# Kernel optimization log

Hardware: AMD Instinct MI355X
Metric: run time of the kernel (lower is better)

## Reference

```python
import jax, jax.numpy as jnp
import numpy as np

B, S, HID, NH, HD = 2, 2048, 1024, 16, 64  # batch, seq, hidden, heads, head_dim (1024//NH)
ROPE_THETA = 10000.0
EPS = 1e-5


def _ternary_quantize(w):
    # BitNet b1.58 absmean weight quantization: ternary values + scalar scale.
    s = jnp.mean(jnp.abs(w)) + EPS
    q = jnp.clip(jnp.round(w / s), -1.0, 1.0)
    return q, s


def _rotate_half(x):
    x1, x2 = jnp.split(x, 2, axis=-1)
    return jnp.concatenate((-x2, x1), axis=-1)


def _rope_cos_sin(position_ids, head_dim, dtype):
    inv_freq = 1.0 / (ROPE_THETA ** (jnp.arange(0, head_dim, 2, dtype=jnp.float32) / head_dim))
    freqs = position_ids.astype(jnp.float32)[..., None] * inv_freq  # [b, s, hd/2]
    emb = jnp.concatenate((freqs, freqs), axis=-1)  # [b, s, hd]
    # add head axis -> [b, 1, s, hd]
    return jnp.cos(emb)[:, None].astype(dtype), jnp.sin(emb)[:, None].astype(dtype)


def setup_inputs() -> dict:
    key = jax.random.key(0)
    ks = jax.random.split(key, 5)
    hidden_states = jax.random.normal(ks[0], (B, S, HID), jnp.float32)
    hidden_states_scale = jnp.ones((1,), jnp.float32)
    position_ids = jnp.broadcast_to(jnp.arange(S, dtype=jnp.int32), (B, S))
    wq = jax.random.normal(ks[1], (HID, HID), jnp.float32) * 0.02
    wk = jax.random.normal(ks[2], (HID, HID), jnp.float32) * 0.02
    wv = jax.random.normal(ks[3], (HID, HID), jnp.float32) * 0.02
    wo = jax.random.normal(ks[4], (HID, HID), jnp.float32) * 0.02
    return {"hidden_states": hidden_states, "hidden_states_scale": hidden_states_scale,
            "position_ids": position_ids, "wq": wq, "wk": wk, "wv": wv, "wo": wo}


def reference(hidden_states, hidden_states_scale, position_ids, wq, wk, wv, wo):
    b, s, _ = hidden_states.shape
    hs_scale = hidden_states_scale.reshape(())

    # QuantizedLinear: ternary weight values, scale carried separately.
    wq_q, sq = _ternary_quantize(wq)
    wk_q, sk = _ternary_quantize(wk)
    wv_q, sv = _ternary_quantize(wv)
    wo_q, so = _ternary_quantize(wo)

    # Projections in the quantized-value domain: out = x @ Wq^T, out_scale = x_scale * w_scale
    q = jnp.einsum('bsh,oh->bso', hidden_states, wq_q)
    k = jnp.einsum('bsh,oh->bso', hidden_states, wk_q)
    v = jnp.einsum('bsh,oh->bso', hidden_states, wv_q)
    q_scale = hs_scale * sq
    k_scale = hs_scale * sk
    v_scale = hs_scale * sv

    # [b, nh, s, hd]
    q = q.reshape(b, s, NH, HD).transpose(0, 2, 1, 3)
    k = k.reshape(b, s, NH, HD).transpose(0, 2, 1, 3)
    v = v.reshape(b, s, NH, HD).transpose(0, 2, 1, 3)

    cos, sin = _rope_cos_sin(position_ids, HD, q.dtype)
    q = q * cos + _rotate_half(q) * sin
    k = k * cos + _rotate_half(k) * sin

    # quantized_matmul(Q, qs, K, ks): values multiply, scales multiply (scale unused by softmax,
    # matching the original which softmaxes the quantized-domain scores).
    attn = jnp.einsum('bhqd,bhkd->bhqk', q, k).astype(jnp.float32) * (1.0 / np.sqrt(HD))
    attn = jax.nn.softmax(attn, axis=-1)

    # quantized_matmul(attn, 1.0, V, vs)
    out = jnp.einsum('bhqk,bhkd->bhqd', attn, v.astype(jnp.float32))
    out_scale = 1.0 * v_scale

    out = out.transpose(0, 2, 1, 3).reshape(b, s, HID)
    out = jnp.einsum('bsh,oh->bso', out, wo_q)
    out_scale = out_scale * so
    return out, out_scale
```

## Files before the change

### kernel.cpp

```cpp
#include <hip/hip_runtime.h>
#include <hip/hip_bf16.h>

#define NB 2
#define NS 2048
#define NHID 1024
#define NHEAD 16
#define NHD 64
#define NTOK (NB*NS)
#define WELEM (NHID*NHID)

typedef unsigned short u16;
typedef __attribute__((ext_vector_type(4))) float floatx4;
typedef __attribute__((ext_vector_type(16))) float floatx16;
typedef __attribute__((ext_vector_type(8))) __bf16 bf16x8;
typedef __attribute__((ext_vector_type(8))) unsigned short ushort8;
typedef __attribute__((ext_vector_type(4))) unsigned short ushort4v;
typedef __attribute__((ext_vector_type(2))) unsigned uint2v;

__device__ __forceinline__ u16 f2bf(float f) {
  union { float f; unsigned u; } a; a.f = f;
  unsigned u = a.u;
  unsigned r = (u + 0x7fffu + ((u >> 16) & 1u)) >> 16;
  return (u16)r;
}
__device__ __forceinline__ float bf2f(u16 s) {
  union { unsigned u; float f; } a; a.u = ((unsigned)s) << 16;
  return a.f;
}
__device__ __forceinline__ void gload16(const void* g, void* lds) {
  __builtin_amdgcn_global_load_lds(
      (const __attribute__((address_space(1))) unsigned int*)g,
      (__attribute__((address_space(3))) unsigned int*)lds, 16, 0, 0);
}
__device__ __forceinline__ uint2v pl32(unsigned a, unsigned b) {
  return __builtin_amdgcn_permlane32_swap(a, b, false, false);
}
__device__ __forceinline__ float mergemax(float x) {
  uint2v r = pl32(__float_as_uint(x), __float_as_uint(x));
  return fmaxf(__uint_as_float(r[0]), __uint_as_float(r[1]));
}
__device__ __forceinline__ float mergesum(float x) {
  uint2v r = pl32(__float_as_uint(x), __float_as_uint(x));
  return __uint_as_float(r[0]) + __uint_as_float(r[1]);
}
__device__ __forceinline__ float tmax16(const floatx16& v) {
  float a = fmaxf(fmaxf(fmaxf(v[0], v[1]), fmaxf(v[2], v[3])),
                  fmaxf(fmaxf(v[4], v[5]), fmaxf(v[6], v[7])));
  float b = fmaxf(fmaxf(fmaxf(v[8], v[9]), fmaxf(v[10], v[11])),
                  fmaxf(fmaxf(v[12], v[13]), fmaxf(v[14], v[15])));
  return fmaxf(a, b);
}

__global__ void k_init(double* sums) { if (threadIdx.x < 4) sums[threadIdx.x] = 0.0; }

__global__ void k_abssum(const float* __restrict__ wq, const float* __restrict__ wk,
                         const float* __restrict__ wv, const float* __restrict__ wo,
                         double* __restrict__ sums) {
  const float* srcs[4] = {wq, wk, wv, wo};
  const float* w = srcs[blockIdx.y];
  int idx = (blockIdx.x * 256 + threadIdx.x) * 16;
  float s = 0.f;
#pragma unroll
  for (int j = 0; j < 4; j++) {
    float4 v = *(const float4*)(w + idx + j * 4);
    s += fabsf(v.x) + fabsf(v.y) + fabsf(v.z) + fabsf(v.w);
  }
#pragma unroll
  for (int off = 32; off; off >>= 1) s += __shfl_down(s, off);
  __shared__ float ps[4];
  if ((threadIdx.x & 63) == 0) ps[threadIdx.x >> 6] = s;
  __syncthreads();
  if (threadIdx.x == 0) atomicAdd(&sums[blockIdx.y], (double)(ps[0] + ps[1] + ps[2] + ps[3]));
}

__global__ void k_quantsplit(const float* __restrict__ wq, const float* __restrict__ wk,
                             const float* __restrict__ wv, const float* __restrict__ wo,
                             const double* __restrict__ sums, u16* __restrict__ wt,
                             const float* __restrict__ x,
                             u16* __restrict__ xh, u16* __restrict__ xl) {
  int bid = blockIdx.x;
  if (bid < 4096) {
    const float* srcs[4] = {wq, wk, wv, wo};
    int y = bid >> 10, xb = bid & 1023;
    const float* w = srcs[y];
    u16* dst = wt + y * WELEM;
    float s = (float)(sums[y] / (double)WELEM) + 1e-5f;
    int idx = (xb * 256 + threadIdx.x) * 4;
    float4 v = *(const float4*)(w + idx);
    float f[4] = {v.x, v.y, v.z, v.w};
    union { u16 ss[4]; uint2 u; } O;
#pragma unroll
    for (int j = 0; j < 4; j++) {
      float q = rintf(f[j] / s);
      q = fminf(1.f, fmaxf(-1.f, q));
      O.ss[j] = f2bf(q);
    }
    *(uint2*)(dst + idx) = O.u;
  } else {
    int idx = ((bid - 4096) * 256 + threadIdx.x) * 4;
    float4 v = *(const float4*)(x + idx);
    float f[4] = {v.x, v.y, v.z, v.w};
    union { u16 s[4]; uint2 u; } H, L;
#pragma unroll
    for (int j = 0; j < 4; j++) {
      u16 hb = f2bf(f[j]);
      H.s[j] = hb;
      L.s[j] = f2bf(f[j] - bf2f(hb));
    }
    *(uint2*)(xh + idx) = H.u;
    *(uint2*)(xl + idx) = L.u;
  }
}

template <int MODE>
__global__ __launch_bounds__(256) void k_gemm(
    const u16* __restrict__ Ahi, const u16* __restrict__ Alo,
    const u16* __restrict__ Wt, float* __restrict__ outf,
    u16* __restrict__ qh, u16* __restrict__ ql,
    u16* __restrict__ kh, u16* __restrict__ kl,
    u16* __restrict__ vt) {
  constexpr int BUF = (MODE == 0) ? 24576 : 16384;
  __shared__ __attribute__((aligned(16))) char GSM[2 * BUF];
  const int tid = threadIdx.x;
  const int wave = tid >> 6, lane = tid & 63;
  const int lr = lane & 15, lh = lane >> 4;
  const int bm = blockIdx.x, bn = blockIdx.y, z = blockIdx.z;
  const u16* W = Wt + (MODE == 0 ? z : 3) * WELEM;
  const int wr = wave >> 1, wc = wave & 1;

  floatx4 acc[4][4];
#pragma unroll
  for (int i = 0; i < 4; i++)
#pragma unroll
    for (int j = 0; j < 4; j++) acc[i][j] = (floatx4){0.f, 0.f, 0.f, 0.f};

  const int e0 = tid * 8;
  const int row0 = e0 >> 5, col0 = e0 & 31;

  auto stage = [&](int k0, int nb) {
#pragma unroll
    for (int it = 0; it < 2; ++it) {
      int row = row0 + it * 64;
      gload16(Ahi + (bm * 128 + row) * 1024 + k0 + col0, GSM + nb + it * 4096 + wave * 1024);
      if (MODE == 0)
        gload16(Alo + (bm * 128 + row) * 1024 + k0 + col0, GSM + nb + 8192 + it * 4096 + wave * 1024);
      gload16(W + (bn * 128 + row) * 1024 + k0 + col0,
              GSM + nb + (MODE == 0 ? 16384 : 8192) + it * 4096 + wave * 1024);
    }
  };

  stage(0, 0);

  for (int kt = 0; kt < 32; ++kt) {
    __syncthreads();
    const int cb = (kt & 1) * BUF;
    if (kt < 31) stage((kt + 1) * 32, ((kt + 1) & 1) * BUF);

    const u16* Ahp = (const u16*)(GSM + cb);
    const u16* Bp  = (const u16*)(GSM + cb + (MODE == 0 ? 16384 : 8192));
    bf16x8 ah[4], bfr[4];
#pragma unroll
    for (int mi = 0; mi < 4; mi++)
      ah[mi] = *(const bf16x8*)(Ahp + (wr * 64 + mi * 16 + lr) * 32 + lh * 8);
#pragma unroll
    for (int ni = 0; ni < 4; ni++)
      bfr[ni] = *(const bf16x8*)(Bp + (wc * 64 + ni * 16 + lr) * 32 + lh * 8);
#pragma unroll
    for (int mi = 0; mi < 4; mi++)
#pragma unroll
      for (int ni = 0; ni < 4; ni++)
        acc[mi][ni] = __builtin_amdgcn_mfma_f32_16x16x32_bf16(ah[mi], bfr[ni], acc[mi][ni], 0, 0, 0);
    if (MODE == 0) {
      const u16* Alp = (const u16*)(GSM + cb + 8192);
      bf16x8 al8[4];
#pragma unroll
      for (int mi = 0; mi < 4; mi++)
        al8[mi] = *(const bf16x8*)(Alp + (wr * 64 + mi * 16 + lr) * 32 + lh * 8);
#pragma unroll
      for (int mi = 0; mi < 4; mi++)
#pragma unroll
        for (int ni = 0; ni < 4; ni++)
          acc[mi][ni] = __builtin_amdgcn_mfma_f32_16x16x32_bf16(al8[mi], bfr[ni], acc[mi][ni], 0, 0, 0);
    }
  }

  if (MODE == 1) {
#pragma unroll
    for (int mi = 0; mi < 4; mi++)
#pragma unroll
      for (int ni = 0; ni < 4; ni++)
#pragma unroll
        for (int i = 0; i < 4; i++) {
          int row = bm * 128 + wr * 64 + mi * 16 + lh * 4 + i;
          int col = bn * 128 + wc * 64 + ni * 16 + lr;
          outf[row * 1024 + col] = acc[mi][ni][i];
        }
    return;
  }

  const int hh = bn * 2 + wc;
  if (z == 2) {
#pragma unroll
    for (int mi = 0; mi < 4; mi++) {
      int row0v = bm * 128 + wr * 64 + mi * 16 + lh * 4;
      int bb = row0v >> 11, s_ = row0v & 2047;
      size_t vbase = ((size_t)(bb * NHEAD + hh)) * (NHD * NS) + s_;
#pragma unroll
      for (int ni = 0; ni < 4; ni++) {
        int hd = ni * 16 + lr;
        union { u16 s4[4]; ushort4v v; } V4;
#pragma unroll
        for (int i = 0; i < 4; i++) V4.s4[i] = f2bf(acc[mi][ni][i]);
        *(ushort4v*)(vt + vbase + (size_t)hd * NS) = V4.v;
      }
    }
    return;
  }

  u16* dh = z ? kh : qh;
  u16* dl = z ? kl : ql;
#pragma unroll
  for (int mi = 0; mi < 4; mi++)
#pragma unroll
    for (int ni = 0; ni < 4; ni++)
#pragma unroll
      for (int i = 0; i < 4; i++) {
        int row = bm * 128 + wr * 64 + mi * 16 + lh * 4 + i;
        int hd = ni * 16 + lr;
        int bb = row >> 11, s_ = row & 2047;
        size_t dst = ((size_t)(bb * NHEAD + hh) * NS + s_) * NHD + hd;
        float v = acc[mi][ni][i];
        u16 hb = f2bf(v);
        dh[dst] = hb;
        dl[dst] = f2bf(v - bf2f(hb));
      }
}

__global__ void k_rope(const int* __restrict__ pos_ids,
                       u16* __restrict__ qh, u16* __restrict__ ql,
                       u16* __restrict__ kh, u16* __restrict__ kl) {
  int gid = blockIdx.x * 256 + threadIdx.x;
  int row = gid >> 5, d = gid & 31;
  int bh = row >> 11, s = row & 2047, b = bh >> 4;
  int pos = pos_ids[b * NS + s];
  float inv = exp2f((float)d * -0.4152410118609203f);
  float fr = (float)pos * inv;
  float c = cosf(fr), sn = sinf(fr);
  int off = row * 64 + d;
  {
    float x1 = bf2f(qh[off]) + bf2f(ql[off]);
    float x2 = bf2f(qh[off + 32]) + bf2f(ql[off + 32]);
    float n1 = x1 * c - x2 * sn;
    float n2 = x2 * c + x1 * sn;
    u16 h1 = f2bf(n1); qh[off] = h1;       ql[off] = f2bf(n1 - bf2f(h1));
    u16 h2 = f2bf(n2); qh[off + 32] = h2;  ql[off + 32] = f2bf(n2 - bf2f(h2));
  }
  {
    float x1 = bf2f(kh[off]) + bf2f(kl[off]);
    float x2 = bf2f(kh[off + 32]) + bf2f(kl[off + 32]);
    float n1 = x1 * c - x2 * sn;
    float n2 = x2 * c + x1 * sn;
    u16 h1 = f2bf(n1); kh[off] = h1;       kl[off] = f2bf(n1 - bf2f(h1));
    u16 h2 = f2bf(n2); kh[off + 32] = h2;  kl[off + 32] = f2bf(n2 - bf2f(h2));
  }
}

__global__ __launch_bounds__(512) void k_attn(
    const u16* __restrict__ qh, const u16* __restrict__ ql,
    const u16* __restrict__ kh, const u16* __restrict__ kl,
    const u16* __restrict__ vt, u16* __restrict__ aoh) {
  __shared__ __attribute__((aligned(16))) char SM[49152];
  const int tid = threadIdx.x, wave = tid >> 6, lane = tid & 63;
  const int l5 = lane & 31, hi = lane >> 5;
  const int bid = blockIdx.x;
  const int swzb = ((bid & 7) << 5) | (bid >> 3);
  const int qt = swzb & 7, bh = swzb >> 3;
  const int b = bh >> 4, hco = (bh & 15) * NHD;
  const int base = bh * (NS * NHD);
  const int qrow = qt * 256 + wave * 32 + l5;
  const float SC = 0.125f * 1.4426950408889634f;

  bf16x8 qfh[4], qfl[4];
#pragma unroll
  for (int s = 0; s < 4; s++) {
    int off = base + qrow * NHD + s * 16 + hi * 8;
    ushort8 hu = *(const ushort8*)(qh + off);
    ushort8 lu = *(const ushort8*)(ql + off);
    union { ushort8 u; bf16x8 v; } H, L;
#pragma unroll
    for (int j = 0; j < 8; j++) {
      float f = (bf2f(hu[j]) + bf2f(lu[j])) * SC;
      u16 hb = f2bf(f);
      H.u[j] = hb; L.u[j] = f2bf(f - bf2f(hb));
    }
    qfh[s] = H.v; qfl[s] = L.v;
  }

  const floatx16 Z16 = {};
  floatx16 acco[2];
  acco[0] = Z16; acco[1] = Z16;
  float m_r = -1e30f, l_r = 0.f;

  const char* khg0 = (const char*)(kh + base);
  const char* klg0 = (const char*)(kl + base);
  const char* vtg0 = (const char*)(vt + base);

#define STAGE_KV(key0_, nb_)                                                     \
  {                                                                              \
    const char* khg = khg0 + (key0_) * 128;                                      \
    const char* klg = klg0 + (key0_) * 128;                                      \
    const char* vtg = vtg0 + (key0_) * 2;                                        \
    int L = tid * 16;                                                            \
    int r7 = (L >> 7) & 7;                                                       \
    int g = L ^ (r7 << 4);                                                       \
    gload16(khg + g, SM + (nb_) + wave * 1024);                                  \
    gload16(klg + g, SM + (nb_) + 8192 + wave * 1024);                           \
    int vcol = (L & 127) ^ (r7 << 4);                                            \
    gload16(vtg + (size_t)(L >> 7) * 4096 + vcol,                                \
            SM + (nb_) + 16384 + wave * 1024);                                   \
  }

  STAGE_KV(0, 0);

  for (int kt = 0; kt < 32; ++kt) {
    __syncthreads();
    const int cb = (kt & 1) * 24576;
    const int key0 = kt * 64;

    if (kt < 31) STAGE_KV(key0 + 64, ((kt + 1) & 1) * 24576);

    floatx16 sacc[2];
#pragma unroll
    for (int t = 0; t < 2; t++) {
      const int row = 32 * t + l5;
      const int swz = (row & 7) << 4;
      {
        int byt = cb + row * 128 + ((hi * 16) ^ swz);
        bf16x8 ah = *(const bf16x8*)(SM + byt);
        bf16x8 al8 = *(const bf16x8*)(SM + 8192 + byt);
        __builtin_amdgcn_s_setprio(1);
        sacc[t] = __builtin_amdgcn_mfma_f32_32x32x16_bf16(ah, qfh[0], Z16, 0, 0, 0);
        sacc[t] = __builtin_amdgcn_mfma_f32_32x32x16_bf16(ah, qfl[0], sacc[t], 0, 0, 0);
        sacc[t] = __builtin_amdgcn_mfma_f32_32x32x16_bf16(al8, qfh[0], sacc[t], 0, 0, 0);
        __builtin_amdgcn_s_setprio(0);
      }
#pragma unroll
      for (int s = 1; s < 4; s++) {
        int byt = cb + row * 128 + ((s * 32 + hi * 16) ^ swz);
        bf16x8 ah = *(const bf16x8*)(SM + byt);
        bf16x8 al8 = *(const bf16x8*)(SM + 8192 + byt);
        __builtin_amdgcn_s_setprio(1);
        sacc[t] = __builtin_amdgcn_mfma_f32_32x32x16_bf16(ah, qfh[s], sacc[t], 0, 0, 0);
        sacc[t] = __builtin_amdgcn_mfma_f32_32x32x16_bf16(ah, qfl[s], sacc[t], 0, 0, 0);
        sacc[t] = __builtin_amdgcn_mfma_f32_32x32x16_bf16(al8, qfh[s], sacc[t], 0, 0, 0);
        __builtin_amdgcn_s_setprio(0);
      }
    }

    float mt = fmaxf(tmax16(sacc[0]), tmax16(sacc[1]));
    mt = mergemax(mt);
    if (!__all(mt <= m_r + 8.0f)) {
      float mn = fmaxf(m_r, mt);
      float sc2 = exp2f(m_r - mn);
      l_r *= sc2;
#pragma unroll
      for (int dt = 0; dt < 2; dt++)
#pragma unroll
        for (int r = 0; r < 16; r++) acco[dt][r] *= sc2;
      m_r = mn;
    }
    float s0 = 0.f, s1 = 0.f, s2 = 0.f, s3 = 0.f;
#pragma unroll
    for (int t = 0; t < 2; t++)
#pragma unroll
      for (int r = 0; r < 16; r += 4) {
        float p0 = exp2f(sacc[t][r + 0] - m_r);
        float p1 = exp2f(sacc[t][r + 1] - m_r);
        float p2 = exp2f(sacc[t][r + 2] - m_r);
        float p3 = exp2f(sacc[t][r + 3] - m_r);
        sacc[t][r + 0] = p0; sacc[t][r + 1] = p1;
        sacc[t][r + 2] = p2; sacc[t][r + 3] = p3;
        s0 += p0; s1 += p1; s2 += p2; s3 += p3;
      }
    l_r += mergesum((s0 + s1) + (s2 + s3));

    bf16x8 vtf[2][4];
#pragma unroll
    for (int dt = 0; dt < 2; dt++) {
      const int vrow = l5 + 32 * dt;
      const int swzv = (vrow & 7) << 4;
#pragma unroll
      for (int s = 0; s < 4; s++)
        vtf[dt][s] = *(const bf16x8*)(SM + cb + 16384 + vrow * 128 + ((s * 32 + hi * 16) ^ swzv));
    }

#pragma unroll
    for (int s = 0; s < 4; s++) {
      int t = s >> 1, rb = (s & 1) * 8;
      union { __bf16 bb[8]; unsigned u[4]; } Wp;
#pragma unroll
      for (int j = 0; j < 8; j++) Wp.bb[j] = (__bf16)sacc[t][rb + j];
      uint2v r02 = pl32(Wp.u[0], Wp.u[2]);
      uint2v r13 = pl32(Wp.u[1], Wp.u[3]);
      union { unsigned u[4]; bf16x8 v; } P;
      P.u[0] = r02[0]; P.u[1] = r13[0]; P.u[2] = r02[1]; P.u[3] = r13[1];
      __builtin_amdgcn_s_setprio(1);
      acco[0] = __builtin_amdgcn_mfma_f32_32x32x16_bf16(vtf[0][s], P.v, acco[0], 0, 0, 0);
      acco[1] = __builtin_amdgcn_mfma_f32_32x32x16_bf16(vtf[1][s], P.v, acco[1], 0, 0, 0);
      __builtin_amdgcn_s_setprio(0);
    }
  }

  float inv = 1.0f / l_r;
  float* OT = (float*)SM;
#pragma unroll
  for (int rnd = 0; rnd < 2; rnd++) {
    __syncthreads();
    if ((wave >> 2) == rnd) {
      int orow = (wave & 3) * 32 + l5;
#pragma unroll
      for (int dt = 0; dt < 2; dt++)
#pragma unroll
        for (int r = 0; r < 16; r++) {
          int col = (r & 3) + 8 * (r >> 2) + 4 * hi + 32 * dt;
          int cs = (col & 32) | ((col ^ l5) & 31);
          OT[orow * 64 + cs] = acco[dt][r] * inv;
        }
    }
    __syncthreads();
    {
      int row = tid >> 2, q4 = tid & 3;
      union { u16 s8[8]; ushort8 v; } HB[2];
#pragma unroll
      for (int j = 0; j < 16; j++) {
        int c = q4 * 16 + j;
        int cs = (c & 32) | ((c ^ (row & 31)) & 31);
        HB[j >> 3].s8[j & 7] = f2bf(OT[row * 64 + cs]);
      }
      int rowg = qt * 256 + rnd * 128 + row;
      size_t doff = ((size_t)(b * NS + rowg)) * NHID + hco + q4 * 16;
      *(ushort8*)(aoh + doff) = HB[0].v;
      *(ushort8*)(aoh + doff + 8) = HB[1].v;
    }
  }
}

__global__ void k_scale(const double* __restrict__ sums, const float* __restrict__ hss,
                        float* __restrict__ out) {
  if (threadIdx.x == 0) {
    float sv = (float)(sums[2] / (double)WELEM) + 1e-5f;
    float so = (float)(sums[3] / (double)WELEM) + 1e-5f;
    out[NTOK * NHID] = hss[0] * sv * so;
  }
}

extern "C" void kernel_launch(void* const* d_in, const int* in_sizes, int n_in,
                              void* d_out, int out_size, void* d_ws, size_t ws_size,
                              hipStream_t stream) {
  const float* x   = (const float*)d_in[0];
  const float* hss = (const float*)d_in[1];
  const int*   pos = (const int*)d_in[2];
  const float* wq  = (const float*)d_in[3];
  const float* wk  = (const float*)d_in[4];
  const float* wv  = (const float*)d_in[5];
  const float* wo  = (const float*)d_in[6];
  float* out = (float*)d_out;
  char* ws = (char*)d_ws;
  const size_t MB = 1u << 20;
  u16* wt = (u16*)(ws);
  u16* xh = (u16*)(ws + 8 * MB);
  u16* xl = (u16*)(ws + 16 * MB);
  u16* qh = (u16*)(ws + 24 * MB);
  u16* ql = (u16*)(ws + 32 * MB);
  u16* kh = (u16*)(ws + 40 * MB);
  u16* kl = (u16*)(ws + 48 * MB);
  u16* vt = (u16*)(ws + 56 * MB);
  double* sums = (double*)(ws + 72 * MB);
  u16* aoh = xh;

  k_init<<<1, 64, 0, stream>>>(sums);
  k_abssum<<<dim3(256, 4), 256, 0, stream>>>(wq, wk, wv, wo, sums);
  k_quantsplit<<<8192, 256, 0, stream>>>(wq, wk, wv, wo, sums, wt, x, xh, xl);
  k_gemm<0><<<dim3(32, 8, 3), 256, 0, stream>>>(xh, xl, wt, nullptr,
                                                qh, ql, kh, kl, vt);
  k_rope<<<8192, 256, 0, stream>>>(pos, qh, ql, kh, kl);
  k_attn<<<256, 512, 0, stream>>>(qh, ql, kh, kl, vt, aoh);
  k_gemm<1><<<dim3(32, 8, 1), 256, 0, stream>>>(aoh, nullptr, wt, out,
                                                nullptr, nullptr, nullptr, nullptr, nullptr);
  k_scale<<<1, 64, 0, stream>>>(sums, hss, out);
}
```

Baseline: 214.3 us.

## Fuse RoPE and query scaling into QKV GEMM epilogue with precomputed table

Removes the standalone RoPE kernel by applying the rotation (and the softmax scale for Q) directly on GEMM accumulators before writing the hi/lo bf16 split. A cos/sin table indexed by position is built inside the existing quantize launch with extra blocks. The attention kernel then loads pre-scaled Q directly instead of re-splitting it. This eliminates a full read-modify-write pass over Q and K, but assumes positions fit the 2048-entry table.

```diff
diff --git a/kernel.cpp b/kernel.cpp
--- a/kernel.cpp
+++ b/kernel.cpp
@@ -77,7 +77,8 @@
                              const float* __restrict__ wv, const float* __restrict__ wo,
                              const double* __restrict__ sums, u16* __restrict__ wt,
                              const float* __restrict__ x,
-                             u16* __restrict__ xh, u16* __restrict__ xl) {
+                             u16* __restrict__ xh, u16* __restrict__ xl,
+                             float2* __restrict__ rtab) {
   int bid = blockIdx.x;
   if (bid < 4096) {
     const float* srcs[4] = {wq, wk, wv, wo};
@@ -96,7 +97,7 @@
       O.ss[j] = f2bf(q);
     }
     *(uint2*)(dst + idx) = O.u;
-  } else {
+  } else if (bid < 8192) {
     int idx = ((bid - 4096) * 256 + threadIdx.x) * 4;
     float4 v = *(const float4*)(x + idx);
     float f[4] = {v.x, v.y, v.z, v.w};
@@ -109,13 +110,21 @@
     }
     *(uint2*)(xh + idx) = H.u;
     *(uint2*)(xl + idx) = L.u;
+  } else {
+    int idx = (bid - 8192) * 256 + threadIdx.x;
+    int d = idx & 31;
+    float p = (float)(idx >> 5);
+    float inv = exp2f((float)d * -0.4152410118609203f);
+    float fr = p * inv;
+    rtab[idx] = make_float2(cosf(fr), sinf(fr));
   }
 }
 
 template <int MODE>
 __global__ __launch_bounds__(256) void k_gemm(
     const u16* __restrict__ Ahi, const u16* __restrict__ Alo,
-    const u16* __restrict__ Wt, float* __restrict__ outf,
+    const u16* __restrict__ Wt, const int* __restrict__ pos_ids,
+    const float2* __restrict__ rtab, float* __restrict__ outf,
     u16* __restrict__ qh, u16* __restrict__ ql,
     u16* __restrict__ kh, u16* __restrict__ kl,
     u16* __restrict__ vt) {
@@ -217,51 +226,36 @@
     return;
   }
 
+  const float qsc = (z == 0) ? 0.125f * 1.4426950408889634f : 1.0f;
   u16* dh = z ? kh : qh;
   u16* dl = z ? kl : ql;
+  int posr[4][4];
 #pragma unroll
   for (int mi = 0; mi < 4; mi++)
 #pragma unroll
-    for (int ni = 0; ni < 4; ni++)
+    for (int i = 0; i < 4; i++) {
+      int row = bm * 128 + wr * 64 + mi * 16 + lh * 4 + i;
+      posr[mi][i] = pos_ids[(row >> 11) * NS + (row & 2047)];
+    }
+#pragma unroll
+  for (int ni = 0; ni < 2; ni++) {
+    int d = ni * 16 + lr;
+#pragma unroll
+    for (int mi = 0; mi < 4; mi++)
 #pragma unroll
       for (int i = 0; i < 4; i++) {
         int row = bm * 128 + wr * 64 + mi * 16 + lh * 4 + i;
-        int hd = ni * 16 + lr;
         int bb = row >> 11, s_ = row & 2047;
-        size_t dst = ((size_t)(bb * NHEAD + hh) * NS + s_) * NHD + hd;
-        float v = acc[mi][ni][i];
-        u16 hb = f2bf(v);
-        dh[dst] = hb;
-        dl[dst] = f2bf(v - bf2f(hb));
-      }
-}
-
-__global__ void k_rope(const int* __restrict__ pos_ids,
-                       u16* __restrict__ qh, u16* __restrict__ ql,
-                       u16* __restrict__ kh, u16* __restrict__ kl) {
-  int gid = blockIdx.x * 256 + threadIdx.x;
-  int row = gid >> 5, d = gid & 31;
-  int bh = row >> 11, s = row & 2047, b = bh >> 4;
-  int pos = pos_ids[b * NS + s];
-  float inv = exp2f((float)d * -0.4152410118609203f);
-  float fr = (float)pos * inv;
-  float c = cosf(fr), sn = sinf(fr);
-  int off = row * 64 + d;
-  {
-    float x1 = bf2f(qh[off]) + bf2f(ql[off]);
-    float x2 = bf2f(qh[off + 32]) + bf2f(ql[off + 32]);
-    float n1 = x1 * c - x2 * sn;
-    float n2 = x2 * c + x1 * sn;
-    u16 h1 = f2bf(n1); qh[off] = h1;       ql[off] = f2bf(n1 - bf2f(h1));
-    u16 h2 = f2bf(n2); qh[off + 32] = h2;  ql[off + 32] = f2bf(n2 - bf2f(h2));
-  }
-  {
-    float x1 = bf2f(kh[off]) + bf2f(kl[off]);
-    float x2 = bf2f(kh[off + 32]) + bf2f(kl[off + 32]);
-    float n1 = x1 * c - x2 * sn;
-    float n2 = x2 * c + x1 * sn;
-    u16 h1 = f2bf(n1); kh[off] = h1;       kl[off] = f2bf(n1 - bf2f(h1));
-    u16 h2 = f2bf(n2); kh[off + 32] = h2;  kl[off + 32] = f2bf(n2 - bf2f(h2));
+        float2 cs = rtab[posr[mi][i] * 32 + d];
+        float x1 = acc[mi][ni][i], x2 = acc[mi][ni + 2][i];
+        float n1 = (x1 * cs.x - x2 * cs.y) * qsc;
+        float n2 = (x2 * cs.x + x1 * cs.y) * qsc;
+        size_t ob = ((size_t)(bb * NHEAD + hh) * NS + s_) * NHD + d;
+        u16 h1 = f2bf(n1);
+        dh[ob] = h1;      dl[ob] = f2bf(n1 - bf2f(h1));
+        u16 h2 = f2bf(n2);
+        dh[ob + 32] = h2; dl[ob + 32] = f2bf(n2 - bf2f(h2));
+      }
   }
 }
 
@@ -278,22 +272,13 @@
   const int b = bh >> 4, hco = (bh & 15) * NHD;
   const int base = bh * (NS * NHD);
   const int qrow = qt * 256 + wave * 32 + l5;
-  const float SC = 0.125f * 1.4426950408889634f;
 
   bf16x8 qfh[4], qfl[4];
 #pragma unroll
   for (int s = 0; s < 4; s++) {
     int off = base + qrow * NHD + s * 16 + hi * 8;
-    ushort8 hu = *(const ushort8*)(qh + off);
-    ushort8 lu = *(const ushort8*)(ql + off);
-    union { ushort8 u; bf16x8 v; } H, L;
-#pragma unroll
-    for (int j = 0; j < 8; j++) {
-      float f = (bf2f(hu[j]) + bf2f(lu[j])) * SC;
-      u16 hb = f2bf(f);
-      H.u[j] = hb; L.u[j] = f2bf(f - bf2f(hb));
-    }
-    qfh[s] = H.v; qfl[s] = L.v;
+    qfh[s] = *(const bf16x8*)(qh + off);
+    qfl[s] = *(const bf16x8*)(ql + off);
   }
 
   const floatx16 Z16 = {};
@@ -476,16 +461,16 @@
   u16* kl = (u16*)(ws + 48 * MB);
   u16* vt = (u16*)(ws + 56 * MB);
   double* sums = (double*)(ws + 72 * MB);
+  float2* rtab = (float2*)(ws + 73 * MB);
   u16* aoh = xh;
 
   k_init<<<1, 64, 0, stream>>>(sums);
   k_abssum<<<dim3(256, 4), 256, 0, stream>>>(wq, wk, wv, wo, sums);
-  k_quantsplit<<<8192, 256, 0, stream>>>(wq, wk, wv, wo, sums, wt, x, xh, xl);
-  k_gemm<0><<<dim3(32, 8, 3), 256, 0, stream>>>(xh, xl, wt, nullptr,
+  k_quantsplit<<<8448, 256, 0, stream>>>(wq, wk, wv, wo, sums, wt, x, xh, xl, rtab);
+  k_gemm<0><<<dim3(32, 8, 3), 256, 0, stream>>>(xh, xl, wt, pos, rtab, nullptr,
                                                 qh, ql, kh, kl, vt);
-  k_rope<<<8192, 256, 0, stream>>>(pos, qh, ql, kh, kl);
   k_attn<<<256, 512, 0, stream>>>(qh, ql, kh, kl, vt, aoh);
-  k_gemm<1><<<dim3(32, 8, 1), 256, 0, stream>>>(aoh, nullptr, wt, out,
+  k_gemm<1><<<dim3(32, 8, 1), 256, 0, stream>>>(aoh, nullptr, wt, nullptr, nullptr, out,
                                                 nullptr, nullptr, nullptr, nullptr, nullptr);
   k_scale<<<1, 64, 0, stream>>>(sums, hss, out);
 }
```

New measurement: 204.1 us. 1.05x faster.
